# Kernel tuning notes

Hardware: AMD Instinct MI355X
Metric: run time of the kernel (lower is better)

## Reference

```python
import jax, jax.numpy as jnp
import numpy as np

TEMPERATURE = 1.0        # sample_codebook_temperature
COMMITMENT_COST = 1.0

B, T, D, K = 8, 4096, 64, 1024


def setup_inputs() -> dict:
    key = jax.random.key(0)
    k1, k2 = jax.random.split(key)
    x = jax.random.normal(k1, (B, T, D), dtype=jnp.float32)
    embeddings = jax.random.normal(k2, (D, K), dtype=jnp.float32)  # (embedding_dim, codebook_size)
    return {"x": x, "embeddings": embeddings}


def gumbel_softmax(logits, temperature):
    # logits: [N, K]
    K_ = logits.shape[1]
    indices = jnp.argmax(logits, axis=1)
    enc = jax.nn.one_hot(indices, K_, dtype=logits.dtype)
    pi0 = jax.nn.softmax(logits, axis=-1)
    pi1 = (enc + jax.nn.softmax(logits / temperature, axis=-1)) / 2
    pi1 = jax.nn.softmax(jax.lax.stop_gradient(jnp.log(pi1) - logits), axis=1)
    pi2 = 2 * pi1 - 0.5 * pi0
    encodings = pi2 - jax.lax.stop_gradient(pi2) + enc  # straight-through encodings
    return indices, encodings


def reference(x, embeddings):
    D_, K_ = embeddings.shape
    flat = x.reshape(-1, D_)                              # [N, D]
    # squared euclidean distances via matmul (cdist trick)
    sim = flat @ embeddings                               # [N, K]
    dist = (jnp.sum(flat ** 2, axis=1, keepdims=True)
            - 2.0 * sim
            + jnp.sum(embeddings ** 2, axis=0, keepdims=True))
    indices, encodings = gumbel_softmax(-dist, TEMPERATURE)
    indices = indices.reshape(x.shape[:-1])               # [B, T]
    quantized = embeddings.T[indices]                     # gather: [B, T, D]
    e_latent_loss = jnp.mean(jnp.square(jax.lax.stop_gradient(quantized) - x))
    loss = e_latent_loss * COMMITMENT_COST
    # straight-through estimator (training-mode output; same values as eval)
    quantized = x + jax.lax.stop_gradient(quantized - x)
    return quantized, encodings, indices, loss
```

## Files before the change

### kernel.cpp

```cpp
#include <hip/hip_runtime.h>
#include <hip/hip_bf16.h>


#define NROWS 32768
#define DDIM  64
#define KCB   1024
#define NSEG  8
#define SEG   128

typedef float f32x4 __attribute__((ext_vector_type(4)));

#define WS_ET    0
#define WS_H     65536
#define WS_PART  66560
#define WS_PBEST 68608
#define WS_PIDX  330752

__global__ __launch_bounds__(256) void k1_prep(const float* __restrict__ E,
                                               float* __restrict__ Et,
                                               float* __restrict__ h) {
  int k = blockIdx.x * 256 + threadIdx.x;
  float col[DDIM];
  float sum = 0.f;
#pragma unroll
  for (int d = 0; d < DDIM; ++d) {
    float v = E[d * KCB + k];
    col[d] = v;
    sum = fmaf(v, v, sum);
  }
  float4* dst = (float4*)(Et + (size_t)k * DDIM);
#pragma unroll
  for (int i = 0; i < 16; ++i)
    dst[i] = make_float4(col[4*i], col[4*i+1], col[4*i+2], col[4*i+3]);
  h[k] = 0.5f * sum;
}

__global__ __launch_bounds__(256, 3) void k2_score(const float* __restrict__ x,
                                                   const float* __restrict__ Et,
                                                   const float* __restrict__ h,
                                                   float* __restrict__ pbest,
                                                   unsigned short* __restrict__ pidx) {
  __shared__ float se[SEG * DDIM];
  __shared__ float sh[SEG];

  int bid = blockIdx.x;
  int ks  = bid >> 7;
  int tid = threadIdx.x;
  int n   = (bid & 127) * 256 + tid;

  {
    const float4* src = (const float4*)(Et + (size_t)ks * SEG * DDIM);
    float4* dst = (float4*)se;
#pragma unroll
    for (int i = 0; i < 8; ++i) dst[tid + i * 256] = src[tid + i * 256];
    if (tid < SEG) sh[tid] = h[ks * SEG + tid];
  }

  const float4* xr = (const float4*)(x + (size_t)n * DDIM);
  float4 xv[16];
#pragma unroll
  for (int i = 0; i < 16; ++i) xv[i] = xr[i];
#pragma unroll
  for (int i = 0; i < 16; ++i)
    asm volatile("" : "+v"(xv[i].x), "+v"(xv[i].y), "+v"(xv[i].z), "+v"(xv[i].w));
  __syncthreads();

  float best = -3.0e38f;
  int besti = ks * SEG;

#pragma unroll 1
  for (int kg = 0; kg < SEG; kg += 8) {
    float acc[8];
#pragma unroll
    for (int j = 0; j < 8; ++j) acc[j] = -sh[kg + j];
#pragma unroll
    for (int i = 0; i < 16; ++i) {
      float4 xi = xv[i];
#pragma unroll
      for (int j = 0; j < 8; ++j) {
        float4 e4 = *(const float4*)(se + (kg + j) * DDIM + i * 4);
        acc[j] = fmaf(xi.x, e4.x, acc[j]);
        acc[j] = fmaf(xi.y, e4.y, acc[j]);
        acc[j] = fmaf(xi.z, e4.z, acc[j]);
        acc[j] = fmaf(xi.w, e4.w, acc[j]);
      }
    }
#pragma unroll
    for (int j = 0; j < 8; ++j) {
      if (acc[j] > best) { best = acc[j]; besti = ks * SEG + kg + j; }
    }
  }
  pbest[ks * NROWS + n] = best;
  pidx [ks * NROWS + n] = (unsigned short)besti;
}

__global__ __launch_bounds__(256) void k34_fused(const float* __restrict__ x,
                                                 const float* __restrict__ Et,
                                                 const float* __restrict__ pbest,
                                                 const unsigned short* __restrict__ pidx,
                                                 float* __restrict__ partial,
                                                 float* __restrict__ out_q,
                                                 float* __restrict__ out_enc,
                                                 float* __restrict__ out_ind) {
  __shared__ int sidx[16];
  int tid = threadIdx.x;
  int r0 = blockIdx.x * 16;

  if (tid < 16) {
    int n = r0 + tid;
    float best = pbest[n];
    int bi = pidx[n];
#pragma unroll
    for (int q = 1; q < NSEG; ++q) {
      float b = pbest[q * NROWS + n];
      int i2 = (int)pidx[q * NROWS + n];
      if (b > best) { best = b; bi = i2; }
    }
    sidx[tid] = bi;
    out_ind[n] = (float)bi;
  }
  __syncthreads();

  int r = tid >> 4, c = tid & 15;
  int n = r0 + r;
  int bi = sidx[r];
  float4 q4 = *(const float4*)(Et + (size_t)bi * DDIM + c * 4);
  float4 x4 = *(const float4*)(x + (size_t)n * DDIM + c * 4);
  float d0 = q4.x - x4.x, d1 = q4.y - x4.y, d2 = q4.z - x4.z, d3 = q4.w - x4.w;
  float lsum = 0.f;
  lsum = fmaf(d0, d0, lsum); lsum = fmaf(d1, d1, lsum);
  lsum = fmaf(d2, d2, lsum); lsum = fmaf(d3, d3, lsum);
  *(float4*)(out_q + (size_t)n * DDIM + c * 4) = q4;

#pragma unroll
  for (int rr = 0; rr < 16; ++rr) {
    int bk = sidx[rr];
    f32x4 v = (f32x4)(0.f);
    if ((bk >> 2) == tid) v[bk & 3] = 1.0f;
    __builtin_nontemporal_store(v, (f32x4*)(out_enc + (size_t)(r0 + rr) * KCB + tid * 4));
  }

#pragma unroll
  for (int off = 32; off > 0; off >>= 1) lsum += __shfl_down(lsum, off);
  __shared__ float red[4];
  int lane = tid & 63, w = tid >> 6;
  if (lane == 0) red[w] = lsum;
  __syncthreads();
  if (tid == 0) partial[blockIdx.x] = red[0] + red[1] + red[2] + red[3];
}

__global__ void k5_loss(const float* __restrict__ partial, float* __restrict__ out_loss) {
  int t = threadIdx.x;
  float s = 0.f;
#pragma unroll
  for (int i = 0; i < 8; ++i) s += partial[t + i * 256];
#pragma unroll
  for (int off = 32; off > 0; off >>= 1) s += __shfl_down(s, off);
  __shared__ float red[4];
  int lane = t & 63, w = t >> 6;
  if (lane == 0) red[w] = s;
  __syncthreads();
  if (t == 0) out_loss[0] = (red[0] + red[1] + red[2] + red[3]) * (1.0f / 2097152.0f);
}

extern "C" void kernel_launch(void* const* d_in, const int* in_sizes, int n_in,
                              void* d_out, int out_size, void* d_ws, size_t ws_size,
                              hipStream_t stream) {
  const float* x = (const float*)d_in[0];
  const float* E = (const float*)d_in[1];

  float* ws    = (float*)d_ws;
  float* Et    = ws + WS_ET;
  float* h     = ws + WS_H;
  float* part  = ws + WS_PART;
  float* pbest = ws + WS_PBEST;
  unsigned short* pidx = (unsigned short*)(ws + WS_PIDX);

  float* out      = (float*)d_out;
  float* out_q    = out;
  float* out_enc  = out + 2097152;
  float* out_ind  = out + 35651584;
  float* out_loss = out + 35684352;

  k1_prep<<<4, 256, 0, stream>>>(E, Et, h);
  k2_score<<<1024, 256, 0, stream>>>(x, Et, h, pbest, pidx);
  k34_fused<<<2048, 256, 0, stream>>>(x, Et, pbest, pidx, part, out_q, out_enc, out_ind);
  k5_loss<<<1, 256, 0, stream>>>(part, out_loss);
}
```

Measured before the change: 236.9 us.

## Register-tile distance kernel with LDS-staged x and codebook tiles

The scoring kernel is restructured from one row per thread (x in registers, codebook read from LDS once per 4 FMAs) into a 64-row by 128-code block tile. Each thread now computes a 4x8 outer-product micro-tile from padded LDS copies of both x and the codebook. The per-row argmax becomes a two-stage reduction through shared memory, with explicit lowest-index tie-breaking, and the merge kernel uses the same tie-break. The aim is to raise FMAs per LDS load. The cost is a 4x larger grid, more LDS per block and an extra reduction phase.

New measurement: 239.7 us. About the same (+1.2%).

```diff
diff --git a/kernel.cpp b/kernel.cpp
--- a/kernel.cpp
+++ b/kernel.cpp
@@ -40,58 +40,101 @@
                                                    const float* __restrict__ h,
                                                    float* __restrict__ pbest,
                                                    unsigned short* __restrict__ pidx) {
-  __shared__ float se[SEG * DDIM];
+  __shared__ float sx[64 * 68];
+  __shared__ float se_[128 * 68];
   __shared__ float sh[SEG];
 
   int bid = blockIdx.x;
-  int ks  = bid >> 7;
+  int ks  = bid >> 9;
+  int rt  = bid & 511;
   int tid = threadIdx.x;
-  int n   = (bid & 127) * 256 + tid;
-
+  int c   = tid & 15;
+  int r   = tid >> 4;
+
+  {
+    const float4* src = (const float4*)(x + (size_t)rt * 64 * DDIM);
+    float4* dst = (float4*)sx;
+#pragma unroll
+    for (int i = 0; i < 4; ++i) {
+      int f = tid + i * 256;
+      dst[(f >> 4) * 17 + (f & 15)] = src[f];
+    }
+  }
   {
     const float4* src = (const float4*)(Et + (size_t)ks * SEG * DDIM);
-    float4* dst = (float4*)se;
-#pragma unroll
-    for (int i = 0; i < 8; ++i) dst[tid + i * 256] = src[tid + i * 256];
-    if (tid < SEG) sh[tid] = h[ks * SEG + tid];
-  }
-
-  const float4* xr = (const float4*)(x + (size_t)n * DDIM);
-  float4 xv[16];
-#pragma unroll
-  for (int i = 0; i < 16; ++i) xv[i] = xr[i];
-#pragma unroll
-  for (int i = 0; i < 16; ++i)
-    asm volatile("" : "+v"(xv[i].x), "+v"(xv[i].y), "+v"(xv[i].z), "+v"(xv[i].w));
-  __syncthreads();
-
-  float best = -3.0e38f;
-  int besti = ks * SEG;
-
-#pragma unroll 1
-  for (int kg = 0; kg < SEG; kg += 8) {
-    float acc[8];
-#pragma unroll
-    for (int j = 0; j < 8; ++j) acc[j] = -sh[kg + j];
-#pragma unroll
-    for (int i = 0; i < 16; ++i) {
-      float4 xi = xv[i];
+    float4* dst = (float4*)se_;
+#pragma unroll
+    for (int i = 0; i < 8; ++i) {
+      int f = tid + i * 256;
+      dst[(f >> 4) * 17 + (f & 15)] = src[f];
+    }
+  }
+  if (tid < SEG) sh[tid] = h[ks * SEG + tid];
+  __syncthreads();
+
+  float acc[4][8];
+#pragma unroll
+  for (int m = 0; m < 4; ++m)
+#pragma unroll
+    for (int j = 0; j < 8; ++j) acc[m][j] = -sh[c + 16 * j];
+
+  const float4* sxf = (const float4*)sx;
+  const float4* sef = (const float4*)se_;
+
+#pragma unroll 2
+  for (int kk = 0; kk < 16; ++kk) {
+    float4 xv[4], ev[8];
+#pragma unroll
+    for (int m = 0; m < 4; ++m) xv[m] = sxf[(r + 16 * m) * 17 + kk];
+#pragma unroll
+    for (int j = 0; j < 8; ++j) ev[j] = sef[(c + 16 * j) * 17 + kk];
+#pragma unroll
+    for (int m = 0; m < 4; ++m) {
 #pragma unroll
       for (int j = 0; j < 8; ++j) {
-        float4 e4 = *(const float4*)(se + (kg + j) * DDIM + i * 4);
-        acc[j] = fmaf(xi.x, e4.x, acc[j]);
-        acc[j] = fmaf(xi.y, e4.y, acc[j]);
-        acc[j] = fmaf(xi.z, e4.z, acc[j]);
-        acc[j] = fmaf(xi.w, e4.w, acc[j]);
+        float a = acc[m][j];
+        a = fmaf(xv[m].x, ev[j].x, a);
+        a = fmaf(xv[m].y, ev[j].y, a);
+        a = fmaf(xv[m].z, ev[j].z, a);
+        a = fmaf(xv[m].w, ev[j].w, a);
+        acc[m][j] = a;
       }
     }
-#pragma unroll
-    for (int j = 0; j < 8; ++j) {
-      if (acc[j] > best) { best = acc[j]; besti = ks * SEG + kg + j; }
-    }
-  }
-  pbest[ks * NROWS + n] = best;
-  pidx [ks * NROWS + n] = (unsigned short)besti;
+  }
+  __syncthreads();
+
+  float* sbest = se_;
+  int*   sidxv = (int*)(se_ + 64 * 17);
+
+#pragma unroll
+  for (int m = 0; m < 4; ++m) {
+    float bm = acc[m][0];
+    int   im = c;
+#pragma unroll
+    for (int j = 1; j < 8; ++j) {
+      int code = c + 16 * j;
+      if (acc[m][j] > bm || (acc[m][j] == bm && code < im)) { bm = acc[m][j]; im = code; }
+    }
+    int row = r + 16 * m;
+    sbest[row * 17 + c] = bm;
+    sidxv[row * 17 + c] = im;
+  }
+  __syncthreads();
+
+  if (tid < 64) {
+    int row = tid;
+    float b = sbest[row * 17];
+    int  ic = sidxv[row * 17];
+#pragma unroll
+    for (int cc = 1; cc < 16; ++cc) {
+      float b2 = sbest[row * 17 + cc];
+      int   i2 = sidxv[row * 17 + cc];
+      if (b2 > b || (b2 == b && i2 < ic)) { b = b2; ic = i2; }
+    }
+    int n = rt * 64 + row;
+    pbest[ks * NROWS + n] = b;
+    pidx [ks * NROWS + n] = (unsigned short)(ks * SEG + ic);
+  }
 }
 
 __global__ __launch_bounds__(256) void k34_fused(const float* __restrict__ x,
@@ -114,23 +157,23 @@
     for (int q = 1; q < NSEG; ++q) {
       float b = pbest[q * NROWS + n];
       int i2 = (int)pidx[q * NROWS + n];
-      if (b > best) { best = b; bi = i2; }
+      if (b > best || (b == best && i2 < bi)) { best = b; bi = i2; }
     }
     sidx[tid] = bi;
     out_ind[n] = (float)bi;
   }
   __syncthreads();
 
-  int r = tid >> 4, c = tid & 15;
+  int r = tid >> 4, cc = tid & 15;
   int n = r0 + r;
   int bi = sidx[r];
-  float4 q4 = *(const float4*)(Et + (size_t)bi * DDIM + c * 4);
-  float4 x4 = *(const float4*)(x + (size_t)n * DDIM + c * 4);
+  float4 q4 = *(const float4*)(Et + (size_t)bi * DDIM + cc * 4);
+  float4 x4 = *(const float4*)(x + (size_t)n * DDIM + cc * 4);
   float d0 = q4.x - x4.x, d1 = q4.y - x4.y, d2 = q4.z - x4.z, d3 = q4.w - x4.w;
   float lsum = 0.f;
   lsum = fmaf(d0, d0, lsum); lsum = fmaf(d1, d1, lsum);
   lsum = fmaf(d2, d2, lsum); lsum = fmaf(d3, d3, lsum);
-  *(float4*)(out_q + (size_t)n * DDIM + c * 4) = q4;
+  *(float4*)(out_q + (size_t)n * DDIM + cc * 4) = q4;
 
 #pragma unroll
   for (int rr = 0; rr < 16; ++rr) {
@@ -183,7 +226,7 @@
   float* out_loss = out + 35684352;
 
   k1_prep<<<4, 256, 0, stream>>>(E, Et, h);
-  k2_score<<<1024, 256, 0, stream>>>(x, Et, h, pbest, pidx);
+  k2_score<<<4096, 256, 0, stream>>>(x, Et, h, pbest, pidx);
   k34_fused<<<2048, 256, 0, stream>>>(x, Et, pbest, pidx, part, out_q, out_enc, out_ind);
   k5_loss<<<1, 256, 0, stream>>>(part, out_loss);
 }
```

## Score codebook with split-fp16 MFMA and rescan near-tie rows in fp32

Applied to the files above, without the earlier changes.

Replaces the fp32 FMA scoring kernel with an MFMA kernel that splits x and the codebook into fp16 hi/lo parts and uses three products per tile to approximate fp32 dot products. It tracks the best and second-best scores per row. Rows whose margin is at most 0.02 are appended to a list through an atomic counter and rescored exactly in fp32 by a separate kernel. This moves the dominant distance matmul onto matrix cores and drops the 8-segment partial-best merge. In exchange it adds a rescan pass, an atomic, and a tie-handling threshold that must hold for argmax exactness.

Result: no change. 241.5 us (+1.9%).

```diff
diff --git a/kernel.cpp b/kernel.cpp
--- a/kernel.cpp
+++ b/kernel.cpp
@@ -5,20 +5,25 @@
 #define NROWS 32768
 #define DDIM  64
 #define KCB   1024
-#define NSEG  8
-#define SEG   128
-
-typedef float f32x4 __attribute__((ext_vector_type(4)));
+
+typedef float    f32x4  __attribute__((ext_vector_type(4)));
+typedef _Float16 f16x8  __attribute__((ext_vector_type(8)));
 
 #define WS_ET    0
 #define WS_H     65536
 #define WS_PART  66560
-#define WS_PBEST 68608
-#define WS_PIDX  330752
+#define WS_IBEST 68608
+#define WS_LIST  101376
+#define WS_CTR   134144
+#define WS_EHI   134148
+#define WS_ELO   166916
 
 __global__ __launch_bounds__(256) void k1_prep(const float* __restrict__ E,
                                                float* __restrict__ Et,
-                                               float* __restrict__ h) {
+                                               float* __restrict__ h,
+                                               _Float16* __restrict__ Ehi,
+                                               _Float16* __restrict__ Elo,
+                                               int* __restrict__ ctr) {
   int k = blockIdx.x * 256 + threadIdx.x;
   float col[DDIM];
   float sum = 0.f;
@@ -33,71 +38,178 @@
   for (int i = 0; i < 16; ++i)
     dst[i] = make_float4(col[4*i], col[4*i+1], col[4*i+2], col[4*i+3]);
   h[k] = 0.5f * sum;
-}
-
-__global__ __launch_bounds__(256, 3) void k2_score(const float* __restrict__ x,
-                                                   const float* __restrict__ Et,
-                                                   const float* __restrict__ h,
-                                                   float* __restrict__ pbest,
-                                                   unsigned short* __restrict__ pidx) {
-  __shared__ float se[SEG * DDIM];
-  __shared__ float sh[SEG];
-
-  int bid = blockIdx.x;
-  int ks  = bid >> 7;
+
+#pragma unroll
+  for (int w = 0; w < 2; ++w) {
+#pragma unroll
+    for (int p = 0; p < 32; ++p) {
+      int dl = w * 32 + 4 * (p >> 3) + (p & 3) + 16 * ((p >> 2) & 1);
+      float v = col[dl];
+      _Float16 hi = (_Float16)v;
+      _Float16 lo = (_Float16)(v - (float)hi);
+      Ehi[(size_t)k * DDIM + w * 32 + p] = hi;
+      Elo[(size_t)k * DDIM + w * 32 + p] = lo;
+    }
+  }
+  if (k == 0) ctr[0] = 0;
+}
+
+__global__ __launch_bounds__(256, 4) void k2_coarse(const float* __restrict__ x,
+                                                    const _Float16* __restrict__ Ehi,
+                                                    const _Float16* __restrict__ Elo,
+                                                    const float* __restrict__ h,
+                                                    int* __restrict__ ibest,
+                                                    int* __restrict__ ctr,
+                                                    int* __restrict__ list) {
   int tid = threadIdx.x;
-  int n   = (bid & 127) * 256 + tid;
-
-  {
-    const float4* src = (const float4*)(Et + (size_t)ks * SEG * DDIM);
-    float4* dst = (float4*)se;
-#pragma unroll
-    for (int i = 0; i < 8; ++i) dst[tid + i * 256] = src[tid + i * 256];
-    if (tid < SEG) sh[tid] = h[ks * SEG + tid];
-  }
-
-  const float4* xr = (const float4*)(x + (size_t)n * DDIM);
-  float4 xv[16];
-#pragma unroll
-  for (int i = 0; i < 16; ++i) xv[i] = xr[i];
-#pragma unroll
-  for (int i = 0; i < 16; ++i)
-    asm volatile("" : "+v"(xv[i].x), "+v"(xv[i].y), "+v"(xv[i].z), "+v"(xv[i].w));
-  __syncthreads();
-
-  float best = -3.0e38f;
-  int besti = ks * SEG;
-
-#pragma unroll 1
-  for (int kg = 0; kg < SEG; kg += 8) {
-    float acc[8];
-#pragma unroll
-    for (int j = 0; j < 8; ++j) acc[j] = -sh[kg + j];
-#pragma unroll
-    for (int i = 0; i < 16; ++i) {
-      float4 xi = xv[i];
-#pragma unroll
-      for (int j = 0; j < 8; ++j) {
-        float4 e4 = *(const float4*)(se + (kg + j) * DDIM + i * 4);
-        acc[j] = fmaf(xi.x, e4.x, acc[j]);
-        acc[j] = fmaf(xi.y, e4.y, acc[j]);
-        acc[j] = fmaf(xi.z, e4.z, acc[j]);
-        acc[j] = fmaf(xi.w, e4.w, acc[j]);
-      }
-    }
-#pragma unroll
-    for (int j = 0; j < 8; ++j) {
-      if (acc[j] > best) { best = acc[j]; besti = ks * SEG + kg + j; }
-    }
-  }
-  pbest[ks * NROWS + n] = best;
-  pidx [ks * NROWS + n] = (unsigned short)besti;
+  int lane = tid & 63, wid = tid >> 6;
+  int g = lane >> 4, c = lane & 15;
+  int n0 = (blockIdx.x * 4 + wid) * 32;
+
+  f16x8 Ahi[2][2], Alo[2][2];
+#pragma unroll
+  for (int r = 0; r < 2; ++r) {
+    const float* xb = x + (size_t)(n0 + r * 16 + c) * DDIM;
+#pragma unroll
+    for (int w = 0; w < 2; ++w) {
+      f32x4 xa = *(const f32x4*)(xb + w * 32 + 4 * g);
+      f32x4 xc = *(const f32x4*)(xb + w * 32 + 16 + 4 * g);
+#pragma unroll
+      for (int e = 0; e < 4; ++e) {
+        _Float16 hi = (_Float16)xa[e];
+        Ahi[r][w][e] = hi;
+        Alo[r][w][e] = (_Float16)(xa[e] - (float)hi);
+      }
+#pragma unroll
+      for (int e = 0; e < 4; ++e) {
+        _Float16 hi = (_Float16)xc[e];
+        Ahi[r][w][4 + e] = hi;
+        Alo[r][w][4 + e] = (_Float16)(xc[e] - (float)hi);
+      }
+    }
+  }
+
+  float b1[2][4], b2[2][4];
+  int   i1[2][4];
+#pragma unroll
+  for (int r = 0; r < 2; ++r)
+#pragma unroll
+    for (int q = 0; q < 4; ++q) { b1[r][q] = -3.0e38f; b2[r][q] = -3.0e38f; i1[r][q] = 0; }
+
+  const _Float16* peh = Ehi + c * DDIM + g * 8;
+  const _Float16* pel = Elo + c * DDIM + g * 8;
+
+  f16x8 bh0n = *(const f16x8*)(peh);
+  f16x8 bl0n = *(const f16x8*)(pel);
+  f16x8 bh1n = *(const f16x8*)(peh + 32);
+  f16x8 bl1n = *(const f16x8*)(pel + 32);
+  float hn = h[c];
+
+  for (int ch = 0; ch < 64; ++ch) {
+    f16x8 bh0 = bh0n, bl0 = bl0n, bh1 = bh1n, bl1 = bl1n;
+    float hc = hn;
+    if (ch < 63) {
+      size_t off = (size_t)(ch + 1) * 16 * DDIM;
+      bh0n = *(const f16x8*)(peh + off);
+      bl0n = *(const f16x8*)(pel + off);
+      bh1n = *(const f16x8*)(peh + off + 32);
+      bl1n = *(const f16x8*)(pel + off + 32);
+      hn = h[(ch + 1) * 16 + c];
+    }
+    int code = ch * 16 + c;
+#pragma unroll
+    for (int r = 0; r < 2; ++r) {
+      f32x4 a = { -hc, -hc, -hc, -hc };
+      a = __builtin_amdgcn_mfma_f32_16x16x32_f16(Alo[r][0], bh0, a, 0, 0, 0);
+      a = __builtin_amdgcn_mfma_f32_16x16x32_f16(Ahi[r][0], bl0, a, 0, 0, 0);
+      a = __builtin_amdgcn_mfma_f32_16x16x32_f16(Ahi[r][0], bh0, a, 0, 0, 0);
+      a = __builtin_amdgcn_mfma_f32_16x16x32_f16(Alo[r][1], bh1, a, 0, 0, 0);
+      a = __builtin_amdgcn_mfma_f32_16x16x32_f16(Ahi[r][1], bl1, a, 0, 0, 0);
+      a = __builtin_amdgcn_mfma_f32_16x16x32_f16(Ahi[r][1], bh1, a, 0, 0, 0);
+#pragma unroll
+      for (int q = 0; q < 4; ++q) {
+        float s = a[q];
+        bool gt = s > b1[r][q];
+        b2[r][q] = gt ? b1[r][q] : fmaxf(b2[r][q], s);
+        i1[r][q] = gt ? code : i1[r][q];
+        b1[r][q] = gt ? s : b1[r][q];
+      }
+    }
+  }
+
+#pragma unroll
+  for (int step = 1; step <= 8; step <<= 1) {
+#pragma unroll
+    for (int r = 0; r < 2; ++r)
+#pragma unroll
+      for (int q = 0; q < 4; ++q) {
+        float ob1 = __shfl_xor(b1[r][q], step);
+        int   oi1 = __shfl_xor(i1[r][q], step);
+        float ob2 = __shfl_xor(b2[r][q], step);
+        bool win = (ob1 > b1[r][q]) || (ob1 == b1[r][q] && oi1 < i1[r][q]);
+        float loser = win ? b1[r][q] : ob1;
+        b1[r][q] = win ? ob1 : b1[r][q];
+        i1[r][q] = win ? oi1 : i1[r][q];
+        b2[r][q] = fmaxf(fmaxf(b2[r][q], ob2), loser);
+      }
+  }
+
+  if (c == 0) {
+#pragma unroll
+    for (int r = 0; r < 2; ++r)
+#pragma unroll
+      for (int q = 0; q < 4; ++q) {
+        int row = n0 + r * 16 + 4 * g + q;
+        ibest[row] = i1[r][q];
+        if (b1[r][q] - b2[r][q] <= 0.02f) {
+          int p = atomicAdd(ctr, 1);
+          list[p] = row;
+        }
+      }
+  }
+}
+
+__global__ __launch_bounds__(256) void k2b_rescan(const float* __restrict__ x,
+                                                  const float* __restrict__ Et,
+                                                  const float* __restrict__ h,
+                                                  const int* __restrict__ ctr,
+                                                  const int* __restrict__ list,
+                                                  int* __restrict__ ibest) {
+  int lane = threadIdx.x & 63;
+  int w = blockIdx.x * 4 + (threadIdx.x >> 6);
+  int cnt = ctr[0];
+  for (int i = w; i < cnt; i += 512) {
+    int n = list[i];
+    const f32x4* xr = (const f32x4*)(x + (size_t)n * DDIM);
+    f32x4 xv[16];
+#pragma unroll
+    for (int d = 0; d < 16; ++d) xv[d] = xr[d];
+    float best = -3.0e38f; int bi = 0;
+    for (int j = 0; j < 16; ++j) {
+      int code = j * 64 + lane;
+      const f32x4* er = (const f32x4*)(Et + (size_t)code * DDIM);
+      float acc = -h[code];
+#pragma unroll
+      for (int d = 0; d < 16; ++d) {
+        f32x4 e4 = er[d], x4 = xv[d];
+        acc = fmaf(x4[0], e4[0], acc); acc = fmaf(x4[1], e4[1], acc);
+        acc = fmaf(x4[2], e4[2], acc); acc = fmaf(x4[3], e4[3], acc);
+      }
+      if (acc > best || (acc == best && code < bi)) { best = acc; bi = code; }
+    }
+#pragma unroll
+    for (int step = 1; step <= 32; step <<= 1) {
+      float ob = __shfl_xor(best, step);
+      int   oi = __shfl_xor(bi, step);
+      if (ob > best || (ob == best && oi < bi)) { best = ob; bi = oi; }
+    }
+    if (lane == 0) ibest[n] = bi;
+  }
 }
 
 __global__ __launch_bounds__(256) void k34_fused(const float* __restrict__ x,
                                                  const float* __restrict__ Et,
-                                                 const float* __restrict__ pbest,
-                                                 const unsigned short* __restrict__ pidx,
+                                                 const int* __restrict__ ibest,
                                                  float* __restrict__ partial,
                                                  float* __restrict__ out_q,
                                                  float* __restrict__ out_enc,
@@ -108,29 +220,22 @@
 
   if (tid < 16) {
     int n = r0 + tid;
-    float best = pbest[n];
-    int bi = pidx[n];
-#pragma unroll
-    for (int q = 1; q < NSEG; ++q) {
-      float b = pbest[q * NROWS + n];
-      int i2 = (int)pidx[q * NROWS + n];
-      if (b > best) { best = b; bi = i2; }
-    }
+    int bi = ibest[n];
     sidx[tid] = bi;
     out_ind[n] = (float)bi;
   }
   __syncthreads();
 
-  int r = tid >> 4, c = tid & 15;
+  int r = tid >> 4, cc = tid & 15;
   int n = r0 + r;
   int bi = sidx[r];
-  float4 q4 = *(const float4*)(Et + (size_t)bi * DDIM + c * 4);
-  float4 x4 = *(const float4*)(x + (size_t)n * DDIM + c * 4);
+  float4 q4 = *(const float4*)(Et + (size_t)bi * DDIM + cc * 4);
+  float4 x4 = *(const float4*)(x + (size_t)n * DDIM + cc * 4);
   float d0 = q4.x - x4.x, d1 = q4.y - x4.y, d2 = q4.z - x4.z, d3 = q4.w - x4.w;
   float lsum = 0.f;
   lsum = fmaf(d0, d0, lsum); lsum = fmaf(d1, d1, lsum);
   lsum = fmaf(d2, d2, lsum); lsum = fmaf(d3, d3, lsum);
-  *(float4*)(out_q + (size_t)n * DDIM + c * 4) = q4;
+  *(float4*)(out_q + (size_t)n * DDIM + cc * 4) = q4;
 
 #pragma unroll
   for (int rr = 0; rr < 16; ++rr) {
@@ -143,8 +248,8 @@
 #pragma unroll
   for (int off = 32; off > 0; off >>= 1) lsum += __shfl_down(lsum, off);
   __shared__ float red[4];
-  int lane = tid & 63, w = tid >> 6;
-  if (lane == 0) red[w] = lsum;
+  int lane = tid & 63, wv = tid >> 6;
+  if (lane == 0) red[wv] = lsum;
   __syncthreads();
   if (tid == 0) partial[blockIdx.x] = red[0] + red[1] + red[2] + red[3];
 }
@@ -173,8 +278,11 @@
   float* Et    = ws + WS_ET;
   float* h     = ws + WS_H;
   float* part  = ws + WS_PART;
-  float* pbest = ws + WS_PBEST;
-  unsigned short* pidx = (unsigned short*)(ws + WS_PIDX);
+  int*   ibest = (int*)(ws + WS_IBEST);
+  int*   list  = (int*)(ws + WS_LIST);
+  int*   ctr   = (int*)(ws + WS_CTR);
+  _Float16* Ehi = (_Float16*)(ws + WS_EHI);
+  _Float16* Elo = (_Float16*)(ws + WS_ELO);
 
   float* out      = (float*)d_out;
   float* out_q    = out;
@@ -182,8 +290,9 @@
   float* out_ind  = out + 35651584;
   float* out_loss = out + 35684352;
 
-  k1_prep<<<4, 256, 0, stream>>>(E, Et, h);
-  k2_score<<<1024, 256, 0, stream>>>(x, Et, h, pbest, pidx);
-  k34_fused<<<2048, 256, 0, stream>>>(x, Et, pbest, pidx, part, out_q, out_enc, out_ind);
+  k1_prep<<<4, 256, 0, stream>>>(E, Et, h, Ehi, Elo, ctr);
+  k2_coarse<<<256, 256, 0, stream>>>(x, Ehi, Elo, h, ibest, ctr, list);
+  k2b_rescan<<<128, 256, 0, stream>>>(x, Et, h, ctr, list, ibest);
+  k34_fused<<<2048, 256, 0, stream>>>(x, Et, ibest, part, out_q, out_enc, out_ind);
   k5_loss<<<1, 256, 0, stream>>>(part, out_loss);
 }
```
